# Optimization experiments

Measured on AMD Instinct MI355X. Metric: run time of the kernel, lower is better.

Reference implementation:

```python
import jax, jax.numpy as jnp
import numpy as np
from jax import lax

# ---- quantum-kernel constants: flipped model f = Tr[rho(theta) O(patch)] ----
# rho(theta) = (I + sum_i theta_i P_i)/4 over the 15 non-identity 2-qubit Paulis.
# O(patch)  = (M + M^T)/2 where M is the 3x3 patch zero-padded to 16 and reshaped 4x4.
# Both are linear in their inputs, so precompute A[i,k] = Re Tr[P_i O(e_k)] and
# t0[k] = Tr[O(e_k)] once on the host.

def _pauli_features():
    I = np.eye(2, dtype=np.complex64)
    X = np.array([[0, 1], [1, 0]], np.complex64)
    Y = np.array([[0, -1j], [1j, 0]], np.complex64)
    Z = np.array([[1, 0], [0, -1]], np.complex64)
    singles = [I, X, Y, Z]
    paulis = [np.kron(a, b) for a in singles for b in singles][1:]  # 15 non-identity
    A = np.zeros((15, 9), np.float32)
    t0 = np.zeros((9,), np.float32)
    for k in range(9):
        M = np.zeros((4, 4), np.complex64)
        M.flat[k] = 1.0
        O = (M + M.conj().T) / 2.0
        t0[k] = float(np.real(np.trace(O)))
        for i, P in enumerate(paulis):
            A[i, k] = float(np.real(np.trace(P @ O)))
    return A, t0

_A_NP, _T0_NP = _pauli_features()
STRIDE = 1
PAD = (1, 1)  # (pad_h, pad_w)


def setup_inputs() -> dict:
    key = jax.random.key(0)
    k1, k2, k3 = jax.random.split(key, 3)
    x = jax.random.normal(k1, (32, 16, 128, 128), dtype=jnp.float32)
    weight = jax.random.normal(k2, (64, 16, 15), dtype=jnp.float32)
    bias = jax.random.normal(k3, (64, 1), dtype=jnp.float32)
    return {"x": x, "weight": weight, "bias": bias}


def reference(x, weight, bias):
    B, C, H, W = x.shape
    ph, pw = PAD
    Ho = (H - 3 + 2 * ph) // STRIDE + 1
    Wo = (W - 3 + 2 * pw) // STRIDE + 1
    # im2col: [B, C*9, Ho, Wo], channel-major (C slowest, 3x3 row-major fastest)
    patches = lax.conv_general_dilated_patches(
        x, (3, 3), (STRIDE, STRIDE), ((ph, ph), (pw, pw)))
    patches = patches.reshape(B, C, 9, Ho * Wo)  # [B, C, 9, P]

    A = jnp.asarray(_A_NP)    # [15, 9]
    t0 = jnp.asarray(_T0_NP)  # [9]

    # identity part of rho: sum over in-channels of Tr[O]/4 (weight-independent)
    base = jnp.einsum('k,bckp->bp', t0, patches)            # [B, P]
    # Pauli features Tr[P_i O(patch)] per (channel, patch)
    qf = jnp.einsum('ik,bckp->bcip', A, patches)            # [B, C, 15, P]
    out = (base[:, None, :] + jnp.einsum('oci,bcip->bop', weight, qf)) * 0.25
    out = out + bias                                        # bias [O,1] -> [B,O,P]
    return out.reshape(B, weight.shape[0], Ho, Wo)
```

## Files before the change

### kernel.cpp

```cpp
#include <hip/hip_runtime.h>
#include <hip/hip_bf16.h>


typedef short bf16x8 __attribute__((ext_vector_type(8)));
typedef float f32x4 __attribute__((ext_vector_type(4)));

__device__ __forceinline__ void pauli_entry(int s, int r, int c, float& re, float& im) {
    re = 0.f; im = 0.f;
    if (s == 0)      { if (r == c) re = 1.f; }
    else if (s == 1) { if (r != c) re = 1.f; }
    else if (s == 2) { if (r == 0 && c == 1) im = -1.f; else if (r == 1 && c == 0) im = 1.f; }
    else             { if (r == c) re = (r == 0) ? 1.f : -1.f; }
}

__device__ __forceinline__ float A_entry(int i, int k) {
    int j = i + 1, sa = j >> 2, sb = j & 3;
    int r = k >> 2, c = k & 3;
    float ar, ai, br, bi;
    pauli_entry(sa, r >> 1, c >> 1, ar, ai);
    pauli_entry(sb, r & 1, c & 1, br, bi);
    float re1 = ar * br - ai * bi;
    pauli_entry(sa, c >> 1, r >> 1, ar, ai);
    pauli_entry(sb, c & 1, r & 1, br, bi);
    float re2 = ar * br - ai * bi;
    return 0.5f * (re1 + re2);
}

__device__ __forceinline__ short f2bf(float f) {
    union { float f; unsigned int u; } a; a.f = f;
    unsigned int r = a.u + 0x7fffu + ((a.u >> 16) & 1u);
    return (short)(r >> 16);
}

__device__ __forceinline__ unsigned pk_bf16(float a, float b) {
#if __has_builtin(__builtin_amdgcn_cvt_pk_bf16_f32)
    typedef __bf16 bf2 __attribute__((ext_vector_type(2)));
    bf2 r = __builtin_amdgcn_cvt_pk_bf16_f32(a, b);
    union { bf2 v; unsigned u; } cv; cv.v = r;
    return cv.u;
#else
    union { float f; unsigned u; } x, y; x.f = a; y.f = b;
    unsigned ra = x.u + 0x7fffu + ((x.u >> 16) & 1u);
    unsigned rb = y.u + 0x7fffu + ((y.u >> 16) & 1u);
    return (ra >> 16) | (rb & 0xffff0000u);
#endif
}

__global__ __launch_bounds__(256) void prep_kernel(const float* __restrict__ weight,
                                                   short* __restrict__ afrag) {
    int t = blockIdx.x * 256 + threadIdx.x;
    if (t >= 1280) return;
    int lane = t & 63;
    int mt   = (t >> 6) & 3;
    int ch   = t >> 8;
    int quad = lane >> 4;
    int m    = mt * 16 + (lane & 15);
    short vals[8];
    #pragma unroll
    for (int j = 0; j < 8; ++j) {
        int k = ch * 32 + quad * 8 + j;
        float v = 0.f;
        if (k < 144) {
            int c  = k / 9;
            int k9 = k - 9 * c;
            float acc = (k9 == 0 || k9 == 5) ? 1.f : 0.f;
            const float* w = weight + (m * 16 + c) * 15;
            #pragma unroll
            for (int i = 0; i < 15; ++i) acc += w[i] * A_entry(i, k9);
            v = 0.25f * acc;
        }
        vals[j] = f2bf(v);
    }
    *(bf16x8*)(afrag + t * 8) = *(bf16x8*)vals;
}

__global__ __launch_bounds__(256) void conv_mfma(const float* __restrict__ x,
                                                 const short* __restrict__ afrag,
                                                 const float* __restrict__ bias,
                                                 float* __restrict__ out) {
    __shared__ float sx[16 * 6 * 136];

    const int tid  = threadIdx.x;
    const int h0   = blockIdx.x * 4;
    const int b    = blockIdx.y;
    const int lane = tid & 63;
    const int wave = tid >> 6;
    const int quad = lane >> 4;
    const int nlo  = lane & 15;

    bf16x8 Areg[20];
    #pragma unroll
    for (int i = 0; i < 20; ++i)
        Areg[i] = *(const bf16x8*)(afrag + (i * 64 + lane) * 8);

    const float* xb = x + (size_t)b * 16 * 128 * 128;
    #pragma unroll
    for (int j = 0; j < 12; ++j) {
        int vid = tid + j * 256;
        int row = vid >> 5;
        int v   = vid & 31;
        int c   = row / 6;
        int r   = row - 6 * c;
        int hp  = h0 - 1 + r;
        float4 val = make_float4(0.f, 0.f, 0.f, 0.f);
        if (hp >= 0 && hp < 128)
            val = *(const float4*)(xb + (c * 128 + hp) * 128 + v * 4);
        *(float4*)(sx + row * 136 + 4 + v * 4) = val;
    }
    if (tid < 192) {
        int row = tid >> 1, side = tid & 1;
        *(float4*)(sx + row * 136 + (side ? 132 : 0)) = make_float4(0.f, 0.f, 0.f, 0.f);
    }

    unsigned offp[20];
    #pragma unroll
    for (int ch = 0; ch < 5; ++ch) {
        #pragma unroll
        for (int j2 = 0; j2 < 4; ++j2) {
            unsigned o01[2];
            #pragma unroll
            for (int t = 0; t < 2; ++t) {
                int k = ch * 32 + quad * 8 + j2 * 2 + t;
                if (k >= 144) k = 0;
                int c  = k / 9, r9 = k - 9 * c;
                int kh = r9 / 3, kw = r9 - 3 * kh;
                o01[t] = (unsigned)((c * 6 + wave + kh) * 136 + 3 + kw + nlo);
            }
            offp[ch * 4 + j2] = o01[0] | (o01[1] << 16);
        }
    }
    __syncthreads();

    const int h = h0 + wave;
    #pragma unroll
    for (int np = 0; np < 4; ++np) {
        const int pixadd = np * 32;

        f32x4 acc[2][4];
        #pragma unroll
        for (int mt = 0; mt < 4; ++mt) {
            f32x4 bv = *(const f32x4*)(bias + mt * 16 + quad * 4);
            acc[0][mt] = bv;
            acc[1][mt] = bv;
        }

        #pragma unroll
        for (int ch = 0; ch < 5; ++ch) {
            unsigned b0p[4], b1p[4];
            #pragma unroll
            for (int j2 = 0; j2 < 4; ++j2) {
                unsigned pk = offp[ch * 4 + j2];
                const float* p0 = sx + (pk & 0xffffu) + pixadd;
                const float* p1 = sx + (pk >> 16) + pixadd;
                float a0 = p0[0], a1 = p0[16];
                float c0 = p1[0], c1 = p1[16];
                b0p[j2] = pk_bf16(a0, c0);
                b1p[j2] = pk_bf16(a1, c1);
            }
            union { unsigned u[4]; bf16x8 v; } B0, B1;
            #pragma unroll
            for (int j2 = 0; j2 < 4; ++j2) { B0.u[j2] = b0p[j2]; B1.u[j2] = b1p[j2]; }
            #pragma unroll
            for (int mt = 0; mt < 4; ++mt) {
                acc[0][mt] = __builtin_amdgcn_mfma_f32_16x16x32_bf16(Areg[ch * 4 + mt], B0.v, acc[0][mt], 0, 0, 0);
                acc[1][mt] = __builtin_amdgcn_mfma_f32_16x16x32_bf16(Areg[ch * 4 + mt], B1.v, acc[1][mt], 0, 0, 0);
            }
        }

        const int wp = pixadd + nlo;
        #pragma unroll
        for (int mt = 0; mt < 4; ++mt) {
            float* dst = out + (((size_t)b * 64 + mt * 16 + quad * 4) * 128 + h) * 128;
            #pragma unroll
            for (int reg = 0; reg < 4; ++reg) {
                float* d = dst + (size_t)reg * 128 * 128;
                d[wp]      = acc[0][mt][reg];
                d[wp + 16] = acc[1][mt][reg];
            }
        }
    }
}

extern "C" void kernel_launch(void* const* d_in, const int* in_sizes, int n_in,
                              void* d_out, int out_size, void* d_ws, size_t ws_size,
                              hipStream_t stream) {
    const float* x      = (const float*)d_in[0];
    const float* weight = (const float*)d_in[1];
    const float* bias   = (const float*)d_in[2];
    float* out   = (float*)d_out;
    short* afrag = (short*)d_ws;

    prep_kernel<<<5, 256, 0, stream>>>(weight, afrag);
    dim3 grid(32, 32);
    conv_mfma<<<grid, 256, 0, stream>>>(x, afrag, bias, out);
}
```

Before: 174.6 us.

## Stage input as channel-interleaved bf16 in LDS and swap MFMA operand roles

The input tile is converted to bf16 once during the global-to-LDS load, in a pixel-major layout with 16 channels interleaved and a swizzled slot. Each MFMA operand then comes from a single 16-byte LDS read instead of eight scalar fp32 reads plus per-use conversion. The reduction axis is reordered tap-major, and the weights become the B operand, so outputs can be written as float4 vectors along width. Each block now covers 8 output rows (two per wave), halving the grid. The risks are uncoalesced strided global loads during staging (8 channel loads per element) and fewer blocks for occupancy.

```diff
diff --git a/kernel.cpp b/kernel.cpp
--- a/kernel.cpp
+++ b/kernel.cpp
@@ -47,135 +47,122 @@
 }
 
 __global__ __launch_bounds__(256) void prep_kernel(const float* __restrict__ weight,
-                                                   short* __restrict__ afrag) {
+                                                   short* __restrict__ bfrag) {
     int t = blockIdx.x * 256 + threadIdx.x;
     if (t >= 1280) return;
-    int lane = t & 63;
-    int mt   = (t >> 6) & 3;
-    int ch   = t >> 8;
-    int quad = lane >> 4;
-    int m    = mt * 16 + (lane & 15);
+    int lane  = t & 63;
+    int ot    = (t >> 6) & 3;
+    int chunk = t >> 8;
+    int q     = lane >> 4;
+    int o     = ot * 16 + (lane & 15);
     short vals[8];
     #pragma unroll
     for (int j = 0; j < 8; ++j) {
-        int k = ch * 32 + quad * 8 + j;
+        int gk = chunk * 32 + q * 8 + j;
         float v = 0.f;
-        if (k < 144) {
-            int c  = k / 9;
-            int k9 = k - 9 * c;
-            float acc = (k9 == 0 || k9 == 5) ? 1.f : 0.f;
-            const float* w = weight + (m * 16 + c) * 15;
+        if (gk < 144) {
+            int tap = gk >> 4;
+            int c   = gk & 15;
+            float acc = (tap == 0 || tap == 5) ? 1.f : 0.f;
+            const float* w = weight + (o * 16 + c) * 15;
             #pragma unroll
-            for (int i = 0; i < 15; ++i) acc += w[i] * A_entry(i, k9);
+            for (int i = 0; i < 15; ++i) acc += w[i] * A_entry(i, tap);
             v = 0.25f * acc;
         }
         vals[j] = f2bf(v);
     }
-    *(bf16x8*)(afrag + t * 8) = *(bf16x8*)vals;
+    *(bf16x8*)(bfrag + t * 8) = *(bf16x8*)vals;
 }
 
 __global__ __launch_bounds__(256) void conv_mfma(const float* __restrict__ x,
-                                                 const short* __restrict__ afrag,
+                                                 const short* __restrict__ bfrag,
                                                  const float* __restrict__ bias,
                                                  float* __restrict__ out) {
-    __shared__ float sx[16 * 6 * 136];
+    __shared__ short sx[10 * 136 * 16];
 
     const int tid  = threadIdx.x;
-    const int h0   = blockIdx.x * 4;
+    const int h0   = blockIdx.x * 8;
     const int b    = blockIdx.y;
     const int lane = tid & 63;
     const int wave = tid >> 6;
-    const int quad = lane >> 4;
+    const int q    = lane >> 4;
     const int nlo  = lane & 15;
-
-    bf16x8 Areg[20];
-    #pragma unroll
-    for (int i = 0; i < 20; ++i)
-        Areg[i] = *(const bf16x8*)(afrag + (i * 64 + lane) * 8);
 
     const float* xb = x + (size_t)b * 16 * 128 * 128;
     #pragma unroll
-    for (int j = 0; j < 12; ++j) {
-        int vid = tid + j * 256;
-        int row = vid >> 5;
-        int v   = vid & 31;
-        int c   = row / 6;
-        int r   = row - 6 * c;
-        int hp  = h0 - 1 + r;
-        float4 val = make_float4(0.f, 0.f, 0.f, 0.f);
-        if (hp >= 0 && hp < 128)
-            val = *(const float4*)(xb + (c * 128 + hp) * 128 + v * 4);
-        *(float4*)(sx + row * 136 + 4 + v * 4) = val;
-    }
-    if (tid < 192) {
-        int row = tid >> 1, side = tid & 1;
-        *(float4*)(sx + row * 136 + (side ? 132 : 0)) = make_float4(0.f, 0.f, 0.f, 0.f);
+    for (int it = 0; it < 11; ++it) {
+        int pos = tid + it * 256;
+        if (pos < 2720) {
+            int seg = pos / 136;
+            int w   = pos - seg * 136;
+            int row = seg >> 1, chalf = seg & 1;
+            int hp  = h0 - 1 + row;
+            int xw  = w - 4;
+            bool ok = ((unsigned)hp < 128u) && ((unsigned)xw < 128u);
+            const float* src = xb + (size_t)(chalf * 8) * 16384 + hp * 128 + xw;
+            float v[8];
+            #pragma unroll
+            for (int j = 0; j < 8; ++j)
+                v[j] = ok ? src[(size_t)j * 16384] : 0.f;
+            int slot = (chalf ^ (w >> 2)) & 1;
+            unsigned* dst = (unsigned*)sx + (row * 136 + w) * 8 + slot * 4;
+            #pragma unroll
+            for (int j2 = 0; j2 < 4; ++j2)
+                dst[j2] = pk_bf16(v[2 * j2], v[2 * j2 + 1]);
+        }
     }
 
-    unsigned offp[20];
+    bf16x8 Breg[20];
+    #pragma unroll
+    for (int i = 0; i < 20; ++i)
+        Breg[i] = *(const bf16x8*)(bfrag + (i * 64 + lane) * 8);
+    float bv[4];
+    #pragma unroll
+    for (int ot = 0; ot < 4; ++ot) bv[ot] = bias[ot * 16 + nlo];
+
+    int baseA[5];
     #pragma unroll
     for (int ch = 0; ch < 5; ++ch) {
-        #pragma unroll
-        for (int j2 = 0; j2 < 4; ++j2) {
-            unsigned o01[2];
-            #pragma unroll
-            for (int t = 0; t < 2; ++t) {
-                int k = ch * 32 + quad * 8 + j2 * 2 + t;
-                if (k >= 144) k = 0;
-                int c  = k / 9, r9 = k - 9 * c;
-                int kh = r9 / 3, kw = r9 - 3 * kh;
-                o01[t] = (unsigned)((c * 6 + wave + kh) * 136 + 3 + kw + nlo);
-            }
-            offp[ch * 4 + j2] = o01[0] | (o01[1] << 16);
-        }
+        int tap = ch * 2 + (q >> 1);
+        if (tap > 8) tap = 8;
+        int kh = tap / 3, kw = tap - 3 * kh;
+        int chalf = q & 1;
+        int row0  = wave * 2 + kh;
+        int w0    = nlo + kw + 3;
+        int slot  = (chalf ^ (w0 >> 2)) & 1;
+        baseA[ch] = (row0 * 136 + w0) * 16 + slot * 8;
     }
     __syncthreads();
 
-    const int h = h0 + wave;
     #pragma unroll
-    for (int np = 0; np < 4; ++np) {
-        const int pixadd = np * 32;
-
-        f32x4 acc[2][4];
+    for (int rs = 0; rs < 2; ++rs) {
+        const int h = h0 + wave * 2 + rs;
         #pragma unroll
-        for (int mt = 0; mt < 4; ++mt) {
-            f32x4 bv = *(const f32x4*)(bias + mt * 16 + quad * 4);
-            acc[0][mt] = bv;
-            acc[1][mt] = bv;
-        }
-
-        #pragma unroll
-        for (int ch = 0; ch < 5; ++ch) {
-            unsigned b0p[4], b1p[4];
+        for (int np = 0; np < 4; ++np) {
+            f32x4 acc[2][4];
             #pragma unroll
-            for (int j2 = 0; j2 < 4; ++j2) {
-                unsigned pk = offp[ch * 4 + j2];
-                const float* p0 = sx + (pk & 0xffffu) + pixadd;
-                const float* p1 = sx + (pk >> 16) + pixadd;
-                float a0 = p0[0], a1 = p0[16];
-                float c0 = p1[0], c1 = p1[16];
-                b0p[j2] = pk_bf16(a0, c0);
-                b1p[j2] = pk_bf16(a1, c1);
+            for (int ot = 0; ot < 4; ++ot) {
+                f32x4 ini = { bv[ot], bv[ot], bv[ot], bv[ot] };
+                acc[0][ot] = ini;
+                acc[1][ot] = ini;
             }
-            union { unsigned u[4]; bf16x8 v; } B0, B1;
             #pragma unroll
-            for (int j2 = 0; j2 < 4; ++j2) { B0.u[j2] = b0p[j2]; B1.u[j2] = b1p[j2]; }
+            for (int ch = 0; ch < 5; ++ch) {
+                const short* pA = sx + baseA[ch] + rs * 2176 + np * 512;
+                bf16x8 A0 = *(const bf16x8*)(pA);
+                bf16x8 A1 = *(const bf16x8*)(pA + 256);
+                #pragma unroll
+                for (int ot = 0; ot < 4; ++ot) {
+                    acc[0][ot] = __builtin_amdgcn_mfma_f32_16x16x32_bf16(A0, Breg[ch * 4 + ot], acc[0][ot], 0, 0, 0);
+                    acc[1][ot] = __builtin_amdgcn_mfma_f32_16x16x32_bf16(A1, Breg[ch * 4 + ot], acc[1][ot], 0, 0, 0);
+                }
+            }
             #pragma unroll
-            for (int mt = 0; mt < 4; ++mt) {
-                acc[0][mt] = __builtin_amdgcn_mfma_f32_16x16x32_bf16(Areg[ch * 4 + mt], B0.v, acc[0][mt], 0, 0, 0);
-                acc[1][mt] = __builtin_amdgcn_mfma_f32_16x16x32_bf16(Areg[ch * 4 + mt], B1.v, acc[1][mt], 0, 0, 0);
-            }
-        }
-
-        const int wp = pixadd + nlo;
-        #pragma unroll
-        for (int mt = 0; mt < 4; ++mt) {
-            float* dst = out + (((size_t)b * 64 + mt * 16 + quad * 4) * 128 + h) * 128;
-            #pragma unroll
-            for (int reg = 0; reg < 4; ++reg) {
-                float* d = dst + (size_t)reg * 128 * 128;
-                d[wp]      = acc[0][mt][reg];
-                d[wp + 16] = acc[1][mt][reg];
+            for (int ot = 0; ot < 4; ++ot) {
+                float* dst = out + (((size_t)b * 64 + ot * 16 + nlo) * 128 + h) * 128
+                           + np * 32 + q * 4;
+                *(f32x4*)dst        = acc[0][ot];
+                *(f32x4*)(dst + 16) = acc[1][ot];
             }
         }
     }
@@ -188,9 +175,9 @@
     const float* weight = (const float*)d_in[1];
     const float* bias   = (const float*)d_in[2];
     float* out   = (float*)d_out;
-    short* afrag = (short*)d_ws;
+    short* bfrag = (short*)d_ws;
 
-    prep_kernel<<<5, 256, 0, stream>>>(weight, afrag);
-    dim3 grid(32, 32);
-    conv_mfma<<<grid, 256, 0, stream>>>(x, afrag, bias, out);
+    prep_kernel<<<5, 256, 0, stream>>>(weight, bfrag);
+    dim3 grid(16, 32);
+    conv_mfma<<<grid, 256, 0, stream>>>(x, bfrag, bias, out);
 }
```

New measurement: 171.5 us. Within noise of the previous version (-1.8%).
